# Kernel optimization log

Measured on AMD Instinct MI355X. Metric: run time of the kernel, lower is better.

Reference implementation:

```python
import jax, jax.numpy as jnp
import numpy as np

# hyperparameters from init_kwargs
TEMP = 0.05
MOMENTUM = 0.2
ALPHA = 0.9
TEMP_DIST = 0.6
LAMBDA1 = 1.0
LAMBDA2 = 1.0
EPS_CONS = 2.0
NUM_SAMPLES = 8192
NUM_FEATURES = 2048
B = 256
K = 20
EPS = 1e-12


def setup_inputs() -> dict:
    key = jax.random.key(0)
    ks = jax.random.split(key, 8)
    inputs0 = jax.random.normal(ks[0], (B, NUM_FEATURES), dtype=jnp.float32)
    logits0 = jax.random.normal(ks[1], (B, NUM_SAMPLES), dtype=jnp.float32)
    logits1 = jax.random.normal(ks[2], (B, NUM_SAMPLES), dtype=jnp.float32)
    targets = jax.random.randint(ks[3], (B,), 0, NUM_SAMPLES, dtype=jnp.int32)
    indexes = jnp.arange(B, dtype=jnp.int32)  # global idx == batch idx (identity idx2bidx)
    neighbors = jax.random.randint(ks[4], (B, K), 0, B, dtype=jnp.int32)
    neighbor_dists = jax.random.uniform(ks[5], (B, K), dtype=jnp.float32)
    rampup = jnp.ones((), dtype=jnp.float32)
    features = jax.random.normal(ks[6], (NUM_SAMPLES, NUM_FEATURES), dtype=jnp.float32)
    features = features / jnp.linalg.norm(features, axis=1, keepdims=True)
    return {
        'inputs0': inputs0, 'logits0': logits0, 'logits1': logits1,
        'targets': targets, 'indexes': indexes, 'neighbors': neighbors,
        'neighbor_dists': neighbor_dists, 'rampup': rampup, 'features': features,
    }


def reference(inputs0, logits0, logits1, targets, indexes, neighbors,
              neighbor_dists, rampup, features):
    # F.normalize(inputs[0], dim=1)
    x = inputs0 / jnp.maximum(jnp.linalg.norm(inputs0, axis=1, keepdims=True), EPS)

    # CM forward: scores against memory bank, scaled by temperature
    outputs = (x @ features.T) / TEMP                      # [B, S]
    logp = jax.nn.log_softmax(outputs, axis=-1)
    loss_nce = -jnp.mean(jnp.take_along_axis(logp, targets[:, None], axis=1))

    targets_onehot = jax.nn.one_hot(targets, NUM_SAMPLES, dtype=logits0.dtype)

    # neighbor gathering: indexes = arange(B) so idx2bidx is identity; every
    # neighbor in [0,B) passes the `nb in indexes` filter.
    p0 = jax.nn.softmax(logits0, axis=-1)[neighbors]       # [B, K, S]
    p1 = jax.nn.softmax(logits1, axis=-1)[neighbors]       # [B, K, S]
    # loop appends logits0-row then logits1-row per neighbor -> interleave
    p = jnp.stack([p0, p1], axis=2).reshape(B, 2 * K, NUM_SAMPLES)
    d2 = jnp.repeat(neighbor_dists, 2, axis=1)             # [B, 2K] (d,d pairs)
    w = jax.nn.softmax(d2 / TEMP_DIST, axis=1)             # [B, 2K]
    logits_neighbors1 = jnp.einsum('bk,bks->bs', w, p)     # [B, S]

    # KL branch: neighbors with dist <= eps_consistency (all, since eps=2.0)
    mask = (neighbor_dists <= EPS_CONS).astype(p0.dtype)   # [B, K]
    cnt = jnp.maximum(mask.sum(axis=1, keepdims=True), 1.0)
    logits_neighbors1_KL = jnp.einsum('bk,bks->bs', mask, p0) / cnt  # [B, S]

    refined = ALPHA * targets_onehot + (1.0 - ALPHA) * jax.lax.stop_gradient(logits_neighbors1)
    loss_ce = jnp.mean(jnp.sum(-refined * jax.nn.log_softmax(logits0, axis=-1), axis=1))

    # KLDivLoss(logsoftmax(logits1).detach(), target) with batchmean reduction
    lp1 = jax.lax.stop_gradient(jax.nn.log_softmax(logits1, axis=-1))
    t = logits_neighbors1_KL
    kl = jnp.sum(jnp.where(t > 0, t * (jnp.log(jnp.maximum(t, EPS)) - lp1), 0.0)) / B

    # CM momentum memory-bank scatter update (backward side-effect in torch);
    # equivalent to the sequential loop when targets are unique in the batch.
    upd = MOMENTUM * features[targets] + (1.0 - MOMENTUM) * x
    upd = upd / jnp.maximum(jnp.linalg.norm(upd, axis=1, keepdims=True), EPS)
    new_features = features.at[targets].set(upd)

    return (loss_nce, LAMBDA1 * loss_ce, LAMBDA2 * rampup * kl, new_features)
```

## Files before the change

### kernel.cpp

```cpp
#include <hip/hip_runtime.h>
#include <cmath>

#define NB 256
#define NS 8192
#define NF 2048
#define NK 20

typedef _Float16 half8 __attribute__((ext_vector_type(8)));
typedef _Float16 half4 __attribute__((ext_vector_type(4)));
typedef float f32x4 __attribute__((ext_vector_type(4)));

__device__ __forceinline__ void async16(const void* g, void* l) {
  __builtin_amdgcn_global_load_lds(
      (const __attribute__((address_space(1))) unsigned int*)g,
      (__attribute__((address_space(3))) unsigned int*)l, 16, 0, 0);
}

__device__ __forceinline__ float waveSum(float v) {
#pragma unroll
  for (int off = 32; off > 0; off >>= 1) v += __shfl_xor(v, off, 64);
  return v;
}
__device__ __forceinline__ float waveMax(float v) {
#pragma unroll
  for (int off = 32; off > 0; off >>= 1) v = fmaxf(v, __shfl_xor(v, off, 64));
  return v;
}

__global__ __launch_bounds__(256) void prep(
    const float* __restrict__ in0, const float* __restrict__ logits0,
    const float* __restrict__ logits1, _Float16* __restrict__ P,
    _Float16* __restrict__ xh, float* __restrict__ alpha,
    float* __restrict__ mll, float* __restrict__ loss) {
  __shared__ float redA[4], redB[4];
  int tid = threadIdx.x, blk = blockIdx.x;
  int wave = tid >> 6, lane = tid & 63;

  if (blk < 512) {
    if (blk == 0 && tid < 3) loss[tid] = 0.0f;
    int r = blk;
    const float* src = (r < NB) ? logits0 : logits1;
    const float4* row = (const float4*)(src + (size_t)(r & (NB - 1)) * NS);
    float4 v[8];
    float mx = -1e30f;
#pragma unroll
    for (int i = 0; i < 8; ++i) {
      v[i] = row[tid + i * 256];
      mx = fmaxf(mx, fmaxf(fmaxf(v[i].x, v[i].y), fmaxf(v[i].z, v[i].w)));
    }
    float wv = waveMax(mx);
    if (lane == 0) redA[wave] = wv;
    __syncthreads();
    float m = fmaxf(fmaxf(redA[0], redA[1]), fmaxf(redA[2], redA[3]));
    float em = expf(m);
    float se = 0.0f;
    half4* prow = (half4*)(P + (size_t)r * NS);
#pragma unroll
    for (int i = 0; i < 8; ++i) {
      float e0 = expf(v[i].x - m), e1 = expf(v[i].y - m);
      float e2 = expf(v[i].z - m), e3 = expf(v[i].w - m);
      se += (e0 + e1) + (e2 + e3);
      half4 h;
      h[0] = (_Float16)(e0 * em); h[1] = (_Float16)(e1 * em);
      h[2] = (_Float16)(e2 * em); h[3] = (_Float16)(e3 * em);
      prow[tid + i * 256] = h;
    }
    float sw = waveSum(se);
    if (lane == 0) redB[wave] = sw;
    __syncthreads();
    float l = (redB[0] + redB[1]) + (redB[2] + redB[3]);
    if (tid == 0) {
      mll[r] = m + logf(l);
      alpha[r] = 256.0f * expf(-m) / l;
    }
  } else {
    int b = blk - 512;
    const float4* row = (const float4*)(in0 + (size_t)b * NF);
    float4 v0 = row[tid], v1 = row[tid + 256];
    float ss = v0.x * v0.x + v0.y * v0.y + v0.z * v0.z + v0.w * v0.w +
               v1.x * v1.x + v1.y * v1.y + v1.z * v1.z + v1.w * v1.w;
    float w = waveSum(ss);
    if (lane == 0) redA[wave] = w;
    __syncthreads();
    float tot = (redA[0] + redA[1]) + (redA[2] + redA[3]);
    float inv = 1.0f / fmaxf(sqrtf(tot), 1e-12f);
    half4 h0, h1;
    h0[0] = (_Float16)(v0.x * inv); h0[1] = (_Float16)(v0.y * inv);
    h0[2] = (_Float16)(v0.z * inv); h0[3] = (_Float16)(v0.w * inv);
    h1[0] = (_Float16)(v1.x * inv); h1[1] = (_Float16)(v1.y * inv);
    h1[2] = (_Float16)(v1.z * inv); h1[3] = (_Float16)(v1.w * inv);
    ((half4*)(xh + (size_t)b * NF))[tid] = h0;
    ((half4*)(xh + (size_t)b * NF))[tid + 256] = h1;
  }
}

__global__ __launch_bounds__(256) void fused2(
    const _Float16* __restrict__ xh, const float* __restrict__ fB,
    const _Float16* __restrict__ P, const float* __restrict__ alpha,
    const float* __restrict__ mll, const float* __restrict__ logits0,
    const float* __restrict__ logits1, const int* __restrict__ targets,
    const int* __restrict__ neighbors, const float* __restrict__ ndist,
    const float* __restrict__ rampup, float* __restrict__ outF,
    float* __restrict__ pm, float* __restrict__ pl, float* __restrict__ tgt,
    float* __restrict__ out) {
  __shared__ alignas(16) _Float16 As[128 * 64];
  __shared__ alignas(16) _Float16 Bs[32 * 64];
  __shared__ float red[8];
  int tid = threadIdx.x, wave = tid >> 6, lane = tid & 63;
  int quad = lane >> 4, r16 = lane & 15;
  int blk = blockIdx.x;

  if (blk < 512) {
    int by = (blk >> 3) & 1;
    int bx = (blk & 7) | ((blk >> 4) << 3);
    int n0 = bx * 32, m0 = by * 128;
    int brow = tid >> 3, bq = tid & 7;
    const float* bsrc = fB + (size_t)(n0 + brow) * NF + bq * 8;

    float4 fv[2];
    f32x4 acc[2][2] = {};
    fv[0] = *(const float4*)bsrc;
    fv[1] = *(const float4*)(bsrc + 4);

    for (int k0 = 0; k0 < NF; k0 += 64) {
      __builtin_amdgcn_s_barrier();
#pragma unroll
      for (int ss = 0; ss < 4; ++ss) {
        int rl = ss * 32 + (tid >> 3);
        int sc = (tid & 7) ^ (rl & 7);
        async16(xh + (size_t)(m0 + rl) * NF + k0 + sc * 8,
                &As[rl * 64 + (tid & 7) * 8]);
      }
      __builtin_amdgcn_sched_barrier(0);
      {
        half8 hh;
        hh[0] = (_Float16)fv[0].x; hh[1] = (_Float16)fv[0].y;
        hh[2] = (_Float16)fv[0].z; hh[3] = (_Float16)fv[0].w;
        hh[4] = (_Float16)fv[1].x; hh[5] = (_Float16)fv[1].y;
        hh[6] = (_Float16)fv[1].z; hh[7] = (_Float16)fv[1].w;
        *(half8*)&Bs[brow * 64 + ((bq ^ (brow & 7)) << 3)] = hh;
      }
      if (k0 + 64 < NF) {
        fv[0] = *(const float4*)(bsrc + k0 + 64);
        fv[1] = *(const float4*)(bsrc + k0 + 68);
        __builtin_amdgcn_sched_barrier(0);
        asm volatile("s_waitcnt vmcnt(2) lgkmcnt(0)");
      } else {
        __builtin_amdgcn_sched_barrier(0);
        asm volatile("s_waitcnt vmcnt(0) lgkmcnt(0)");
      }
      __builtin_amdgcn_sched_barrier(0);
      __builtin_amdgcn_s_barrier();
#pragma unroll
      for (int sub = 0; sub < 2; ++sub) {
        int slot = ((sub * 4 + quad) ^ (r16 & 7)) * 8;
        half8 af[2], bf[2];
#pragma unroll
        for (int i = 0; i < 2; ++i)
          af[i] = *(const half8*)&As[(wave * 32 + i * 16 + r16) * 64 + slot];
#pragma unroll
        for (int j = 0; j < 2; ++j)
          bf[j] = *(const half8*)&Bs[(j * 16 + r16) * 64 + slot];
#pragma unroll
        for (int i = 0; i < 2; ++i)
#pragma unroll
          for (int j = 0; j < 2; ++j)
            acc[i][j] = __builtin_amdgcn_mfma_f32_16x16x32_f16(af[i], bf[j], acc[i][j], 0, 0, 0);
      }
    }
#pragma unroll
    for (int i = 0; i < 2; ++i)
#pragma unroll
      for (int r = 0; r < 4; ++r) {
        int R = m0 + wave * 32 + i * 16 + quad * 4 + r;
        float s0 = acc[i][0][r] * 20.0f, s1 = acc[i][1][r] * 20.0f;
        float mx = fmaxf(s0, s1);
#pragma unroll
        for (int m2 = 1; m2 < 16; m2 <<= 1) mx = fmaxf(mx, __shfl_xor(mx, m2, 64));
        float e = expf(s0 - mx) + expf(s1 - mx);
#pragma unroll
        for (int m2 = 1; m2 < 16; m2 <<= 1) e += __shfl_xor(e, m2, 64);
        int tg = targets[R];
        if (n0 + r16 == tg) tgt[R] = s0;
        if (n0 + 16 + r16 == tg) tgt[R] = s1;
        if (r16 == 0) { pm[R * 256 + bx] = mx; pl[R * 256 + bx] = e; }
      }
  } else {
    int gb = blk - 512;
    {
      const float4* src = (const float4*)fB + (size_t)gb * 8 * 512;
      float4* dst = (float4*)outF + (size_t)gb * 8 * 512;
#pragma unroll
      for (int i = 0; i < 16; ++i) dst[tid + i * 256] = src[tid + i * 256];
    }
    int b = gb >> 2, s0 = (gb & 3) * 2048;
    float s = 0.0f;
    int cnt = 0;
#pragma unroll
    for (int k = 0; k < NK; ++k) {
      float d = ndist[b * NK + k];
      s += expf(d * (1.0f / 0.6f));
      cnt += (d <= 2.0f) ? 1 : 0;
    }
    float invs = 1.0f / (2.0f * s);
    float invc = 1.0f / fmaxf((float)cnt, 1.0f);
    float ce[8] = {0, 0, 0, 0, 0, 0, 0, 0};
    float kl[8] = {0, 0, 0, 0, 0, 0, 0, 0};
    int sc_ = s0 + tid * 8;
#pragma unroll 4
    for (int k = 0; k < NK; ++k) {
      float d = ndist[b * NK + k];
      int n = neighbors[b * NK + k];
      float wce = expf(d * (1.0f / 0.6f)) * invs;
      float wkl = (d <= 2.0f) ? invc : 0.0f;
      float a0 = alpha[n], a1 = alpha[256 + n];
      float c0 = wce * a0, c1 = wce * a1, ck = wkl * a0;
      half8 p0 = *(const half8*)(P + (size_t)n * NS + sc_);
      half8 p1 = *(const half8*)(P + (size_t)(256 + n) * NS + sc_);
#pragma unroll
      for (int e2 = 0; e2 < 8; ++e2) {
        float q0 = (float)p0[e2], q1 = (float)p1[e2];
        ce[e2] += c0 * q0 + c1 * q1;
        kl[e2] += ck * q0;
      }
    }
    float mv0 = mll[b], mv1 = mll[256 + b];
    const float* g0 = logits0 + (size_t)b * NS + sc_;
    const float* g1 = logits1 + (size_t)b * NS + sc_;
    float4 l0a = *(const float4*)g0, l0b = *(const float4*)(g0 + 4);
    float4 l1a = *(const float4*)g1, l1b = *(const float4*)(g1 + 4);
    float lg0[8] = {l0a.x, l0a.y, l0a.z, l0a.w, l0b.x, l0b.y, l0b.z, l0b.w};
    float lg1[8] = {l1a.x, l1a.y, l1a.z, l1a.w, l1b.x, l1b.y, l1b.z, l1b.w};
    float lce = 0.0f, lkl = 0.0f;
#pragma unroll
    for (int e2 = 0; e2 < 8; ++e2) {
      float t = ce[e2] * (1.0f / 256.0f);
      lce += t * (lg0[e2] - mv0);
      float tk = kl[e2] * (1.0f / 256.0f);
      lkl += (tk > 0.0f) ? tk * (logf(fmaxf(tk, 1e-12f)) - (lg1[e2] - mv1)) : 0.0f;
    }
    float wc = waveSum(lce), wk = waveSum(lkl);
    if (lane == 0) { red[wave] = wc; red[4 + wave] = wk; }
    __syncthreads();
    if (tid == 0) {
      float ce_t = (red[0] + red[1]) + (red[2] + red[3]);
      float kl_t = (red[4] + red[5]) + (red[6] + red[7]);
      atomicAdd(out + 1, -0.1f * ce_t * (1.0f / 256.0f));
      atomicAdd(out + 2, rampup[0] * kl_t * (1.0f / 256.0f));
    }
  }
}

__global__ __launch_bounds__(128) void final_reduce(
    const float* __restrict__ pm, const float* __restrict__ pl,
    const float* __restrict__ tgt, const float* __restrict__ logits0,
    const float* __restrict__ mll, const int* __restrict__ targets,
    const float* __restrict__ in0, const float* __restrict__ features,
    float* __restrict__ outF, float* __restrict__ out) {
  __shared__ float rA[2], rB[2];
  __shared__ int flag;
  int tid = threadIdx.x, blk = blockIdx.x;
  if (blk < 256) {
    int b = blk;
    float m1 = pm[b * 256 + tid], m2v = pm[b * 256 + 128 + tid];
    float l1 = pl[b * 256 + tid], l2v = pl[b * 256 + 128 + tid];
    float wm = waveMax(fmaxf(m1, m2v));
    if ((tid & 63) == 0) rA[tid >> 6] = wm;
    __syncthreads();
    float mx = fmaxf(rA[0], rA[1]);
    float e = l1 * expf(m1 - mx) + l2v * expf(m2v - mx);
    float ws = waveSum(e);
    if ((tid & 63) == 0) rB[tid >> 6] = ws;
    __syncthreads();
    if (tid == 0) {
      float S = rB[0] + rB[1];
      float nce = -(tgt[b] - mx - logf(S));
      int tg = targets[b];
      float oh = -0.9f * (logits0[(size_t)b * NS + tg] - mll[b]);
      atomicAdd(out + 0, nce * (1.0f / 256.0f));
      atomicAdd(out + 1, oh * (1.0f / 256.0f));
    }
  } else {
    int b = blk - 256;
    int tg = targets[b];
    if (tid == 0) flag = 0;
    __syncthreads();
    bool later = false;
    for (int i = b + 1 + tid; i < 256; i += 128) later = later || (targets[i] == tg);
    if (later) flag = 1;
    __syncthreads();
    if (flag) return;
    const float4* xr = (const float4*)(in0 + (size_t)b * NF);
    const float4* fr = (const float4*)(features + (size_t)tg * NF);
    float4 a[4];
    float ssx = 0.0f;
#pragma unroll
    for (int s = 0; s < 4; ++s) {
      a[s] = xr[tid + s * 128];
      ssx += a[s].x * a[s].x + a[s].y * a[s].y + a[s].z * a[s].z + a[s].w * a[s].w;
    }
    float w1 = waveSum(ssx);
    if ((tid & 63) == 0) rA[tid >> 6] = w1;
    __syncthreads();
    float ix = 0.8f / fmaxf(sqrtf(rA[0] + rA[1]), 1e-12f);
    float4 v[4];
    float ss = 0.0f;
#pragma unroll
    for (int s = 0; s < 4; ++s) {
      float4 f = fr[tid + s * 128];
      v[s] = make_float4(0.2f * f.x + ix * a[s].x, 0.2f * f.y + ix * a[s].y,
                         0.2f * f.z + ix * a[s].z, 0.2f * f.w + ix * a[s].w);
      ss += v[s].x * v[s].x + v[s].y * v[s].y + v[s].z * v[s].z + v[s].w * v[s].w;
    }
    float w2 = waveSum(ss);
    if ((tid & 63) == 0) rB[tid >> 6] = w2;
    __syncthreads();
    float inv = 1.0f / fmaxf(sqrtf(rB[0] + rB[1]), 1e-12f);
    float4* o4 = (float4*)(outF + (size_t)tg * NF);
#pragma unroll
    for (int s = 0; s < 4; ++s)
      o4[tid + s * 128] = make_float4(v[s].x * inv, v[s].y * inv, v[s].z * inv, v[s].w * inv);
  }
}

extern "C" void kernel_launch(void* const* d_in, const int* in_sizes, int n_in,
                              void* d_out, int out_size, void* d_ws, size_t ws_size,
                              hipStream_t stream) {
  const float* inputs0 = (const float*)d_in[0];
  const float* logits0 = (const float*)d_in[1];
  const float* logits1 = (const float*)d_in[2];
  const int* targets = (const int*)d_in[3];
  const int* neighbors = (const int*)d_in[5];
  const float* ndist = (const float*)d_in[6];
  const float* rampup = (const float*)d_in[7];
  const float* features = (const float*)d_in[8];
  float* out = (float*)d_out;

  char* ws = (char*)d_ws;
  float* mll = (float*)(ws + 4096);
  float* alpha = (float*)(ws + 8192);
  float* tgt = (float*)(ws + 16384);
  float* pm = (float*)(ws + 65536);
  float* pl = (float*)(ws + 65536 + 262144);
  _Float16* xh = (_Float16*)(ws + (3 << 20));
  _Float16* P = (_Float16*)(ws + (4 << 20));

  prep<<<768, 256, 0, stream>>>(inputs0, logits0, logits1, P, xh, alpha, mll, out);
  fused2<<<1536, 256, 0, stream>>>(xh, features, P, alpha, mll, logits0, logits1,
                                   targets, neighbors, ndist, rampup, out + 3,
                                   pm, pl, tgt, out);
  final_reduce<<<512, 128, 0, stream>>>(pm, pl, tgt, logits0, mll, targets,
                                        inputs0, features, out + 3, out);
}
```

Measured before the change: 199.0 us.

## Keep A tile in registers with split-K waves and 1024-thread blocks

The fused kernel moves to 1024-thread blocks. Each wave now keeps its 16-row slice of normalized x (fp16) in registers for the whole K range, and two wave groups split K and combine partial sums through shared memory. Each GEMM block processes two 32-column feature tiles in sequence, reusing the register-resident A, and prefetches B three steps ahead. The side blocks handle a full batch row and copy 32 feature rows each. The aim is to cut repeated A loads through LDS and halve the block count, at the cost of high register pressure, two barriers per K step and fewer GEMM blocks (256).

```diff
diff --git a/kernel.cpp b/kernel.cpp
--- a/kernel.cpp
+++ b/kernel.cpp
@@ -9,12 +9,6 @@
 typedef _Float16 half8 __attribute__((ext_vector_type(8)));
 typedef _Float16 half4 __attribute__((ext_vector_type(4)));
 typedef float f32x4 __attribute__((ext_vector_type(4)));
-
-__device__ __forceinline__ void async16(const void* g, void* l) {
-  __builtin_amdgcn_global_load_lds(
-      (const __attribute__((address_space(1))) unsigned int*)g,
-      (__attribute__((address_space(3))) unsigned int*)l, 16, 0, 0);
-}
 
 __device__ __forceinline__ float waveSum(float v) {
 #pragma unroll
@@ -94,7 +88,7 @@
   }
 }
 
-__global__ __launch_bounds__(256) void fused2(
+__global__ __launch_bounds__(1024) void fused2(
     const _Float16* __restrict__ xh, const float* __restrict__ fB,
     const _Float16* __restrict__ P, const float* __restrict__ alpha,
     const float* __restrict__ mll, const float* __restrict__ logits0,
@@ -103,97 +97,112 @@
     const float* __restrict__ rampup, float* __restrict__ outF,
     float* __restrict__ pm, float* __restrict__ pl, float* __restrict__ tgt,
     float* __restrict__ out) {
-  __shared__ alignas(16) _Float16 As[128 * 64];
   __shared__ alignas(16) _Float16 Bs[32 * 64];
-  __shared__ float red[8];
+  __shared__ alignas(16) float redf[128][32];
+  __shared__ float red[32];
   int tid = threadIdx.x, wave = tid >> 6, lane = tid & 63;
   int quad = lane >> 4, r16 = lane & 15;
   int blk = blockIdx.x;
 
-  if (blk < 512) {
+  if (blk < 256) {
     int by = (blk >> 3) & 1;
-    int bx = (blk & 7) | ((blk >> 4) << 3);
-    int n0 = bx * 32, m0 = by * 128;
+    int bxp = (blk & 7) | ((blk >> 4) << 3);
+    int m0 = by * 128;
+    int mg = wave >> 1, kg = wave & 1;
+    int arow = m0 + mg * 16 + r16;
     int brow = tid >> 3, bq = tid & 7;
-    const float* bsrc = fB + (size_t)(n0 + brow) * NF + bq * 8;
-
-    float4 fv[2];
-    f32x4 acc[2][2] = {};
-    fv[0] = *(const float4*)bsrc;
-    fv[1] = *(const float4*)(bsrc + 4);
-
-    for (int k0 = 0; k0 < NF; k0 += 64) {
-      __builtin_amdgcn_s_barrier();
-#pragma unroll
-      for (int ss = 0; ss < 4; ++ss) {
-        int rl = ss * 32 + (tid >> 3);
-        int sc = (tid & 7) ^ (rl & 7);
-        async16(xh + (size_t)(m0 + rl) * NF + k0 + sc * 8,
-                &As[rl * 64 + (tid & 7) * 8]);
-      }
-      __builtin_amdgcn_sched_barrier(0);
-      {
-        half8 hh;
-        hh[0] = (_Float16)fv[0].x; hh[1] = (_Float16)fv[0].y;
-        hh[2] = (_Float16)fv[0].z; hh[3] = (_Float16)fv[0].w;
-        hh[4] = (_Float16)fv[1].x; hh[5] = (_Float16)fv[1].y;
-        hh[6] = (_Float16)fv[1].z; hh[7] = (_Float16)fv[1].w;
-        *(half8*)&Bs[brow * 64 + ((bq ^ (brow & 7)) << 3)] = hh;
-      }
-      if (k0 + 64 < NF) {
-        fv[0] = *(const float4*)(bsrc + k0 + 64);
-        fv[1] = *(const float4*)(bsrc + k0 + 68);
+    float4 fvb[3][2];
+    const float* bsrc0 = fB + (size_t)(bxp * 32 + brow) * NF + bq * 8;
+    if (tid < 256) {
+#pragma unroll
+      for (int d = 0; d < 3; ++d) {
+        fvb[d][0] = *(const float4*)(bsrc0 + d * 64);
+        fvb[d][1] = *(const float4*)(bsrc0 + d * 64 + 4);
+      }
+    }
+    __builtin_amdgcn_sched_barrier(0);
+    half8 A[32];
+    const _Float16* asrc = xh + (size_t)arow * NF + kg * 32 + quad * 8;
+#pragma unroll
+    for (int ki = 0; ki < 32; ++ki) A[ki] = *(const half8*)(asrc + ki * 64);
+
+    for (int t = 0; t < 2; ++t) {
+      int bx = bxp + t * 128;
+      int n0 = bx * 32;
+      const float* bsrc = fB + (size_t)(n0 + brow) * NF + bq * 8;
+      if (t > 0 && tid < 256) {
+#pragma unroll
+        for (int d = 0; d < 3; ++d) {
+          fvb[d][0] = *(const float4*)(bsrc + d * 64);
+          fvb[d][1] = *(const float4*)(bsrc + d * 64 + 4);
+        }
+      }
+      f32x4 acc0 = {}, acc1 = {};
+#pragma unroll
+      for (int ki = 0; ki < 32; ++ki) {
+        __builtin_amdgcn_s_barrier();
         __builtin_amdgcn_sched_barrier(0);
-        asm volatile("s_waitcnt vmcnt(2) lgkmcnt(0)");
-      } else {
+        if (tid < 256) {
+          float4 va = fvb[ki % 3][0], vb = fvb[ki % 3][1];
+          half8 hh;
+          hh[0] = (_Float16)va.x; hh[1] = (_Float16)va.y;
+          hh[2] = (_Float16)va.z; hh[3] = (_Float16)va.w;
+          hh[4] = (_Float16)vb.x; hh[5] = (_Float16)vb.y;
+          hh[6] = (_Float16)vb.z; hh[7] = (_Float16)vb.w;
+          *(half8*)&Bs[brow * 64 + ((bq ^ (brow & 7)) << 3)] = hh;
+          if (ki < 29) {
+            fvb[ki % 3][0] = *(const float4*)(bsrc + (ki + 3) * 64);
+            fvb[ki % 3][1] = *(const float4*)(bsrc + (ki + 3) * 64 + 4);
+          }
+        }
         __builtin_amdgcn_sched_barrier(0);
-        asm volatile("s_waitcnt vmcnt(0) lgkmcnt(0)");
-      }
-      __builtin_amdgcn_sched_barrier(0);
-      __builtin_amdgcn_s_barrier();
-#pragma unroll
-      for (int sub = 0; sub < 2; ++sub) {
-        int slot = ((sub * 4 + quad) ^ (r16 & 7)) * 8;
-        half8 af[2], bf[2];
-#pragma unroll
-        for (int i = 0; i < 2; ++i)
-          af[i] = *(const half8*)&As[(wave * 32 + i * 16 + r16) * 64 + slot];
-#pragma unroll
-        for (int j = 0; j < 2; ++j)
-          bf[j] = *(const half8*)&Bs[(j * 16 + r16) * 64 + slot];
-#pragma unroll
-        for (int i = 0; i < 2; ++i)
-#pragma unroll
-          for (int j = 0; j < 2; ++j)
-            acc[i][j] = __builtin_amdgcn_mfma_f32_16x16x32_f16(af[i], bf[j], acc[i][j], 0, 0, 0);
-      }
-    }
-#pragma unroll
-    for (int i = 0; i < 2; ++i)
-#pragma unroll
-      for (int r = 0; r < 4; ++r) {
-        int R = m0 + wave * 32 + i * 16 + quad * 4 + r;
-        float s0 = acc[i][0][r] * 20.0f, s1 = acc[i][1][r] * 20.0f;
-        float mx = fmaxf(s0, s1);
-#pragma unroll
-        for (int m2 = 1; m2 < 16; m2 <<= 1) mx = fmaxf(mx, __shfl_xor(mx, m2, 64));
-        float e = expf(s0 - mx) + expf(s1 - mx);
-#pragma unroll
-        for (int m2 = 1; m2 < 16; m2 <<= 1) e += __shfl_xor(e, m2, 64);
-        int tg = targets[R];
-        if (n0 + r16 == tg) tgt[R] = s0;
-        if (n0 + 16 + r16 == tg) tgt[R] = s1;
-        if (r16 == 0) { pm[R * 256 + bx] = mx; pl[R * 256 + bx] = e; }
-      }
+        asm volatile("s_waitcnt lgkmcnt(0)");
+        __builtin_amdgcn_sched_barrier(0);
+        __builtin_amdgcn_s_barrier();
+        __builtin_amdgcn_sched_barrier(0);
+        int slot = ((kg * 4 + quad) ^ (r16 & 7)) * 8;
+        half8 bf0 = *(const half8*)&Bs[r16 * 64 + slot];
+        half8 bf1 = *(const half8*)&Bs[(16 + r16) * 64 + slot];
+        acc0 = __builtin_amdgcn_mfma_f32_16x16x32_f16(A[ki], bf0, acc0, 0, 0, 0);
+        acc1 = __builtin_amdgcn_mfma_f32_16x16x32_f16(A[ki], bf1, acc1, 0, 0, 0);
+      }
+      if (kg == 1) {
+#pragma unroll
+        for (int r = 0; r < 4; ++r) {
+          redf[mg * 16 + quad * 4 + r][r16] = acc0[r];
+          redf[mg * 16 + quad * 4 + r][16 + r16] = acc1[r];
+        }
+      }
+      __syncthreads();
+      if (kg == 0) {
+#pragma unroll
+        for (int r = 0; r < 4; ++r) {
+          int rr = mg * 16 + quad * 4 + r;
+          float s0 = (acc0[r] + redf[rr][r16]) * 20.0f;
+          float s1 = (acc1[r] + redf[rr][16 + r16]) * 20.0f;
+          float mx = fmaxf(s0, s1);
+#pragma unroll
+          for (int m2 = 1; m2 < 16; m2 <<= 1) mx = fmaxf(mx, __shfl_xor(mx, m2, 64));
+          float e = expf(s0 - mx) + expf(s1 - mx);
+#pragma unroll
+          for (int m2 = 1; m2 < 16; m2 <<= 1) e += __shfl_xor(e, m2, 64);
+          int R = m0 + rr;
+          int tg = targets[R];
+          if (n0 + r16 == tg) tgt[R] = s0;
+          if (n0 + 16 + r16 == tg) tgt[R] = s1;
+          if (r16 == 0) { pm[R * 256 + bx] = mx; pl[R * 256 + bx] = e; }
+        }
+      }
+      __syncthreads();
+    }
   } else {
-    int gb = blk - 512;
+    int b = blk - 256;
     {
-      const float4* src = (const float4*)fB + (size_t)gb * 8 * 512;
-      float4* dst = (float4*)outF + (size_t)gb * 8 * 512;
-#pragma unroll
-      for (int i = 0; i < 16; ++i) dst[tid + i * 256] = src[tid + i * 256];
-    }
-    int b = gb >> 2, s0 = (gb & 3) * 2048;
+      const float4* srcc = (const float4*)fB + (size_t)b * 32 * 512;
+      float4* dstc = (float4*)outF + (size_t)b * 32 * 512;
+#pragma unroll
+      for (int i = 0; i < 16; ++i) dstc[tid + i * 1024] = srcc[tid + i * 1024];
+    }
     float s = 0.0f;
     int cnt = 0;
 #pragma unroll
@@ -206,7 +215,7 @@
     float invc = 1.0f / fmaxf((float)cnt, 1.0f);
     float ce[8] = {0, 0, 0, 0, 0, 0, 0, 0};
     float kl[8] = {0, 0, 0, 0, 0, 0, 0, 0};
-    int sc_ = s0 + tid * 8;
+    int sc_ = tid * 8;
 #pragma unroll 4
     for (int k = 0; k < NK; ++k) {
       float d = ndist[b * NK + k];
@@ -240,11 +249,12 @@
       lkl += (tk > 0.0f) ? tk * (logf(fmaxf(tk, 1e-12f)) - (lg1[e2] - mv1)) : 0.0f;
     }
     float wc = waveSum(lce), wk = waveSum(lkl);
-    if (lane == 0) { red[wave] = wc; red[4 + wave] = wk; }
+    if (lane == 0) { red[wave] = wc; red[16 + wave] = wk; }
     __syncthreads();
     if (tid == 0) {
-      float ce_t = (red[0] + red[1]) + (red[2] + red[3]);
-      float kl_t = (red[4] + red[5]) + (red[6] + red[7]);
+      float ce_t = 0.0f, kl_t = 0.0f;
+#pragma unroll
+      for (int i = 0; i < 16; ++i) { ce_t += red[i]; kl_t += red[16 + i]; }
       atomicAdd(out + 1, -0.1f * ce_t * (1.0f / 256.0f));
       atomicAdd(out + 2, rampup[0] * kl_t * (1.0f / 256.0f));
     }
@@ -346,7 +356,7 @@
   _Float16* P = (_Float16*)(ws + (4 << 20));
 
   prep<<<768, 256, 0, stream>>>(inputs0, logits0, logits1, P, xh, alpha, mll, out);
-  fused2<<<1536, 256, 0, stream>>>(xh, features, P, alpha, mll, logits0, logits1,
+  fused2<<<512, 1024, 0, stream>>>(xh, features, P, alpha, mll, logits0, logits1,
                                    targets, neighbors, ndist, rampup, out + 3,
                                    pm, pl, tgt, out);
   final_reduce<<<512, 128, 0, stream>>>(pm, pl, tgt, logits0, mll, targets,
```

Measured after the change: 263.2 us. 1.32x slower.
